# Kernel optimization log

Measured on AMD Instinct MI355X. Metric: run time of the kernel, lower is better.

## Reference

```python
import jax, jax.numpy as jnp
import numpy as np

B, S, H, N_HEAD = 2, 2048, 1024, 16
NEG = float(-(2 ** 32) + 1)  # -4294967295.0, the module's padding value
EPS = 1e-08


def setup_inputs() -> dict:
    key = jax.random.key(0)
    ks = jax.random.split(key, 11)
    sc = 0.02
    return {
        "queries": jax.random.normal(ks[0], (B, S, H), dtype=jnp.float32),
        "keys": jax.random.normal(ks[1], (B, S, H), dtype=jnp.float32),
        "values": jax.random.normal(ks[2], (B, S, H), dtype=jnp.float32),
        "Wq": jax.random.normal(ks[3], (H, H), dtype=jnp.float32) * sc,
        "bq": jax.random.normal(ks[4], (H,), dtype=jnp.float32) * sc,
        "Wk": jax.random.normal(ks[5], (H, H), dtype=jnp.float32) * sc,
        "bk": jax.random.normal(ks[6], (H,), dtype=jnp.float32) * sc,
        "Wv": jax.random.normal(ks[7], (H, H), dtype=jnp.float32) * sc,
        "bv": jax.random.normal(ks[8], (H,), dtype=jnp.float32) * sc,
        "Wo": jax.random.normal(ks[9], (H, H), dtype=jnp.float32) * sc,
        "bo": jax.random.normal(ks[10], (H,), dtype=jnp.float32) * sc,
    }


def reference(queries, keys, values, Wq, bq, Wk, bk, Wv, bv, Wo, bo):
    n = N_HEAD
    Bb, Sq, Hh = queries.shape
    Sk = keys.shape[1]
    d = Hh // n

    # Linear + ReLU projections
    Q = jax.nn.relu(queries @ Wq + bq)  # [B,Sq,H]
    K = jax.nn.relu(keys @ Wk + bk)     # [B,Sk,H]
    V = jax.nn.relu(values @ Wv + bv)   # [B,Sk,H]

    # chunk(dim=2) + cat(dim=0) == head-major split: [n,B,S,d]
    Q_ = Q.reshape(Bb, Sq, n, d).transpose(2, 0, 1, 3)
    K_ = K.reshape(Bb, Sk, n, d).transpose(2, 0, 1, 3)
    V_ = V.reshape(Bb, Sk, n, d).transpose(2, 0, 1, 3)

    # key padding mask from full (pre-chunk) K: [B,Sk]
    key_masks = jnp.sign(jnp.abs(jnp.sum(K, axis=-1)))

    # scores: [n,B,Sq,Sk], scaled by sqrt(per-head dim)
    scores = jnp.einsum("hbqd,hbkd->hbqk", Q_, K_) / (d ** 0.5)

    # multiplicative padding-mask selection -> equivalent where()
    scores = jnp.where(key_masks[None, :, None, :] == 0.0, NEG, scores)

    # causal tril mask (masked=True)
    tril = jnp.tril(jnp.ones((Sq, Sk), dtype=scores.dtype))
    scores = jnp.where(tril[None, None] == 0.0, NEG, scores)

    attn = jax.nn.softmax(scores, axis=-1)
    out = jnp.einsum("hbqk,hbkd->hbqd", attn, V_)  # [n,B,Sq,d]

    # cat chunks back along feature dim: [B,Sq,H]
    out = out.transpose(1, 2, 0, 3).reshape(Bb, Sq, Hh)

    out = jax.nn.relu(out @ Wo + bo)
    # sublayer connection (dropout treated as identity for determinism)
    out = queries + out

    # layer norm with torch-style unbiased std, gamma=1, beta=0
    mean = out.mean(axis=-1, keepdims=True)
    std = jnp.std(out, axis=-1, ddof=1, keepdims=True)
    return (out - mean) / (std + EPS)
```

## Files before the change

kernel.cpp:

```cpp
#include <hip/hip_runtime.h>
#include <math.h>

typedef __bf16 bf16;
typedef __attribute__((ext_vector_type(8))) __bf16 bf16x8;
typedef __attribute__((ext_vector_type(4))) __bf16 bf16x4;
typedef __attribute__((ext_vector_type(4))) float f32x4;

typedef __attribute__((address_space(1))) unsigned int glb_u32;
typedef __attribute__((address_space(3))) unsigned int lds_u32;

#define NEGV (-4294967295.0f)
#define SCL2 0.18033688011112042f

__device__ __forceinline__ void async_cp16(const void* g, void* l) {
  __builtin_amdgcn_global_load_lds((glb_u32*)g, (lds_u32*)l, 16, 0, 0);
}

template <int CTRL>
__device__ __forceinline__ float dppf(float x) {
  return __builtin_bit_cast(float,
      __builtin_amdgcn_mov_dpp(__builtin_bit_cast(int, x), CTRL, 0xF, 0xF, true));
}
__device__ __forceinline__ float dpp_max16(float x) {
  x = fmaxf(x, dppf<0xB1>(x));
  x = fmaxf(x, dppf<0x4E>(x));
  x = fmaxf(x, dppf<0x141>(x));
  x = fmaxf(x, dppf<0x140>(x));
  return x;
}

__global__ __launch_bounds__(256) void cvt3_kernel(
    const float* __restrict__ q, const float* __restrict__ k,
    const float* __restrict__ v, short* xq, short* xk, short* xv) {
  const int bid = blockIdx.x;
  const int which = bid >> 12;
  const int i = (bid & 4095) * 256 + threadIdx.x;
  const float* src = which == 0 ? q : (which == 1 ? k : v);
  short* dst = which == 0 ? xq : (which == 1 ? xk : xv);
  float4 vv = ((const float4*)src)[i];
  bf16x4 o;
  o[0] = (bf16)vv.x; o[1] = (bf16)vv.y; o[2] = (bf16)vv.z; o[3] = (bf16)vv.w;
  ((bf16x4*)dst)[i] = o;
}

__global__ __launch_bounds__(256) void wt_kernel(
    const float* __restrict__ W0, const float* __restrict__ W1,
    const float* __restrict__ W2, const float* __restrict__ W3,
    short* T0, short* T1, short* T2, short* T3) {
  __shared__ float tile[64][65];
  const float* W = blockIdx.z == 0 ? W0 : (blockIdx.z == 1 ? W1 : (blockIdx.z == 2 ? W2 : W3));
  bf16* T = (bf16*)(blockIdx.z == 0 ? T0 : (blockIdx.z == 1 ? T1 : (blockIdx.z == 2 ? T2 : T3)));
  const int k0 = blockIdx.y * 64, n0 = blockIdx.x * 64;
  const int tid = threadIdx.x;
  const int c = tid & 63, rr = tid >> 6;
#pragma unroll
  for (int i = 0; i < 16; i++) {
    int r = i * 4 + rr;
    tile[r][c] = W[(size_t)(k0 + r) * 1024 + n0 + c];
  }
  __syncthreads();
#pragma unroll
  for (int i = 0; i < 16; i++) {
    int r = i * 4 + rr;
    T[(size_t)(n0 + r) * 1024 + k0 + c] = (bf16)tile[c][r];
  }
}

__global__ __launch_bounds__(256) void qkv_gemm(
    const short* Xq_, const short* Xk_, const short* Xv_,
    const short* Wtq_, const short* Wtk_, const short* Wtv_,
    const float* __restrict__ bq_, const float* __restrict__ bk_, const float* __restrict__ bv_,
    short* Qo_, short* Ko_, short* Vto_) {
  __shared__ bf16 Alds[128][32];
  __shared__ bf16 Blds[128][32];
  const int f = blockIdx.x;
  const int xcd = f & 7, s = f >> 3;
  const int g = xcd + 8 * (s >> 3);
  const int which = g >> 5;
  const int m0 = (g & 31) * 128;
  const int n0 = (s & 7) * 128;
  const bf16* X  = (const bf16*)(which == 0 ? Xq_  : (which == 1 ? Xk_  : Xv_));
  const bf16* Wt = (const bf16*)(which == 0 ? Wtq_ : (which == 1 ? Wtk_ : Wtv_));
  const float* bias = which == 0 ? bq_ : (which == 1 ? bk_ : bv_);
  const int tid = threadIdx.x, wid = tid >> 6, lane = tid & 63;
  const int wr = wid >> 1, wc = wid & 1;
  const int l15 = lane & 15, lg = lane >> 4;
  const f32x4 vzero = {0.f, 0.f, 0.f, 0.f};
  f32x4 acc[4][4];
#pragma unroll
  for (int m = 0; m < 4; m++)
#pragma unroll
    for (int n = 0; n < 4; n++) acc[m][n] = vzero;

  const int sr = wid * 32 + (lane >> 2);
  const int scb = (lane & 3) * 16;

  for (int kt = 0; kt < 32; ++kt) {
    const char* ga = (const char*)(X + (size_t)(m0 + sr) * 1024 + kt * 32) + scb;
    async_cp16(ga, &Alds[wid * 32][0]);
    async_cp16(ga + 16 * 2048, &Alds[wid * 32 + 16][0]);
    const char* gb = (const char*)(Wt + (size_t)(n0 + sr) * 1024 + kt * 32) + scb;
    async_cp16(gb, &Blds[wid * 32][0]);
    async_cp16(gb + 16 * 2048, &Blds[wid * 32 + 16][0]);
    __syncthreads();
    bf16x8 a[4], bb[4];
#pragma unroll
    for (int m = 0; m < 4; m++) a[m] = *(const bf16x8*)&Alds[wr * 64 + m * 16 + l15][lg * 8];
#pragma unroll
    for (int n = 0; n < 4; n++) bb[n] = *(const bf16x8*)&Blds[wc * 64 + n * 16 + l15][lg * 8];
#pragma unroll
    for (int m = 0; m < 4; m++)
#pragma unroll
      for (int n = 0; n < 4; n++)
        acc[m][n] = __builtin_amdgcn_mfma_f32_16x16x32_bf16(a[m], bb[n], acc[m][n], 0, 0, 0);
    __syncthreads();
  }

  if (which != 2) {
    bf16* Y = (bf16*)(which == 0 ? Qo_ : Ko_);
    const float osc = (which == 0) ? SCL2 : 1.0f;
#pragma unroll
    for (int n = 0; n < 4; n++) {
      const int col = n0 + wc * 64 + n * 16 + l15;
      const float bv = bias[col];
#pragma unroll
      for (int m = 0; m < 4; m++) {
        const int row0 = m0 + wr * 64 + m * 16 + lg * 4;
#pragma unroll
        for (int r = 0; r < 4; r++) {
          float v = acc[m][n][r] + bv;
          v = v > 0.f ? v : 0.f;
          Y[(size_t)(row0 + r) * 1024 + col] = (bf16)(v * osc);
        }
      }
    }
  } else {
    bf16* Vt = (bf16*)Vto_;
#pragma unroll
    for (int n = 0; n < 4; n++) {
      const int col = n0 + wc * 64 + n * 16 + l15;
      const float bv = bias[col];
#pragma unroll
      for (int m = 0; m < 4; m++) {
        const int row0 = m0 + wr * 64 + m * 16 + lg * 4;
        const int bb2 = row0 >> 11;
        const int s2 = row0 & 2047;
        bf16x4 pk;
#pragma unroll
        for (int r = 0; r < 4; r++) {
          float v = acc[m][n][r] + bv;
          v = v > 0.f ? v : 0.f;
          pk[r] = (bf16)v;
        }
        *(bf16x4*)(Vt + ((size_t)bb2 * 1024 + col) * 2048 + s2) = pk;
      }
    }
  }
}

__global__ __launch_bounds__(256) void out_gemm(
    const short* A_, const short* Wt_, const float* __restrict__ bias,
    float* __restrict__ Y) {
  __shared__ bf16 Alds[128][32];
  __shared__ bf16 Blds[128][32];
  const bf16* X = (const bf16*)A_;
  const bf16* Wt = (const bf16*)Wt_;
  const int f = blockIdx.x;
  const int xcd = f & 7, s = f >> 3;
  const int g = xcd + 8 * (s >> 3);
  const int m0 = g * 128;
  const int n0 = (s & 7) * 128;
  const int tid = threadIdx.x, wid = tid >> 6, lane = tid & 63;
  const int wr = wid >> 1, wc = wid & 1;
  const int l15 = lane & 15, lg = lane >> 4;
  const f32x4 vzero = {0.f, 0.f, 0.f, 0.f};
  f32x4 acc[4][4];
#pragma unroll
  for (int m = 0; m < 4; m++)
#pragma unroll
    for (int n = 0; n < 4; n++) acc[m][n] = vzero;

  const int sr = wid * 32 + (lane >> 2);
  const int scb = (lane & 3) * 16;

  for (int kt = 0; kt < 32; ++kt) {
    const char* ga = (const char*)(X + (size_t)(m0 + sr) * 1024 + kt * 32) + scb;
    async_cp16(ga, &Alds[wid * 32][0]);
    async_cp16(ga + 16 * 2048, &Alds[wid * 32 + 16][0]);
    const char* gb = (const char*)(Wt + (size_t)(n0 + sr) * 1024 + kt * 32) + scb;
    async_cp16(gb, &Blds[wid * 32][0]);
    async_cp16(gb + 16 * 2048, &Blds[wid * 32 + 16][0]);
    __syncthreads();
    bf16x8 a[4], bb[4];
#pragma unroll
    for (int m = 0; m < 4; m++) a[m] = *(const bf16x8*)&Alds[wr * 64 + m * 16 + l15][lg * 8];
#pragma unroll
    for (int n = 0; n < 4; n++) bb[n] = *(const bf16x8*)&Blds[wc * 64 + n * 16 + l15][lg * 8];
#pragma unroll
    for (int m = 0; m < 4; m++)
#pragma unroll
      for (int n = 0; n < 4; n++)
        acc[m][n] = __builtin_amdgcn_mfma_f32_16x16x32_bf16(a[m], bb[n], acc[m][n], 0, 0, 0);
    __syncthreads();
  }
#pragma unroll
  for (int n = 0; n < 4; n++) {
    const int col = n0 + wc * 64 + n * 16 + l15;
    const float bv = bias[col];
#pragma unroll
    for (int m = 0; m < 4; m++) {
      const int row0 = m0 + wr * 64 + m * 16 + lg * 4;
#pragma unroll
      for (int r = 0; r < 4; r++) {
        float v = acc[m][n][r] + bv;
        Y[(size_t)(row0 + r) * 1024 + col] = v > 0.f ? v : 0.f;
      }
    }
  }
}

__global__ __launch_bounds__(256) void key_mask_kernel(const short* Kb_,
                                                       unsigned* __restrict__ kbits) {
  __shared__ unsigned bits[4];
  const bf16* Kb = (const bf16*)Kb_;
  const int wid = threadIdx.x >> 6, lane = threadIdx.x & 63;
  const int row0 = blockIdx.x * 32 + wid * 8;
  unsigned mybits = 0;
#pragma unroll
  for (int i = 0; i < 8; i++) {
    const bf16x8* p = (const bf16x8*)(Kb + (size_t)(row0 + i) * 1024);
    bf16x8 v0 = p[lane];
    bf16x8 v1 = p[64 + lane];
    float s = 0.f;
#pragma unroll
    for (int jj = 0; jj < 8; jj++) s += (float)v0[jj] + (float)v1[jj];
    for (int m = 32; m; m >>= 1) s += __shfl_xor(s, m);
    if (s != 0.f) mybits |= 1u << (wid * 8 + i);
  }
  if (lane == 0) bits[wid] = mybits;
  __syncthreads();
  if (threadIdx.x == 0) kbits[blockIdx.x] = bits[0] | bits[1] | bits[2] | bits[3];
}

__device__ __forceinline__ bf16x8 lds_read_swz(const bf16* base, int row, int cbyte) {
  return *(const bf16x8*)((const char*)base + row * 128 + (cbyte ^ ((row & 7) << 4)));
}

__global__ __launch_bounds__(128) void attn_kernel(
    const short* Q_, const short* K_, const short* Vt_,
    const unsigned* __restrict__ kbits, short* O_) {
  __shared__ bf16 Klds[2][64][64];
  __shared__ bf16 Vlds[2][64][64];
  __shared__ bf16 Plds[2][16][64];
  const bf16* Q = (const bf16*)Q_;
  const bf16* K = (const bf16*)K_;
  const bf16* Vt = (const bf16*)Vt_;
  bf16* O = (bf16*)O_;

  const int f = blockIdx.x;
  const int xcd = f & 7, idx = f >> 3;
  const int qtb = idx & 31;
  const int hb = xcd + 8 * (idx >> 5);
  const int h = hb & 15, b = hb >> 4;

  const int tid = threadIdx.x, wid = tid >> 6, lane = tid & 63;
  const int l15 = lane & 15, lg = lane >> 4;
  const f32x4 vzero = {0.f, 0.f, 0.f, 0.f};
  bf16* const pbase = &Plds[wid][0][0];

  const int srow = lane >> 3;
  const int cb = (lane & 7) * 16;
  const int cbs = cb ^ ((srow & 7) << 4);

  bf16x8 vones;
#pragma unroll
  for (int i = 0; i < 8; i++) vones[i] = (bf16)1.0f;

  for (int seg = 0; seg < 2; ++seg) {
    const int qt = (seg == 0) ? qtb : 63 - qtb;
    const int q0 = qt * 32;
    const int nkt = (32 * qt + 95) >> 6;

    const int qrow = q0 + wid * 16 + l15;
    const bf16* qp = Q + ((size_t)b * 2048 + qrow) * 1024 + h * 64;
    const bf16x8 qf0 = *(const bf16x8*)(qp + lg * 8);
    const bf16x8 qf1 = *(const bf16x8*)(qp + 32 + lg * 8);

    float Mrow[4];
    f32x4 oacc[4], oaccL;
#pragma unroll
    for (int r = 0; r < 4; r++) Mrow[r] = -INFINITY;
#pragma unroll
    for (int n = 0; n < 4; n++) oacc[n] = vzero;
    oaccL = vzero;
    float Mmin = -INFINITY;

    const char* kn = (const char*)(K + ((size_t)b * 2048 + wid * 32 + srow) * 1024 + h * 64) + cbs;
    const char* vn = (const char*)(Vt + ((size_t)b * 1024 + h * 64 + wid * 32 + srow) * 2048) + cbs;

    auto STAGE = [&](int buf) {
#pragma unroll
      for (int c = 0; c < 4; c++) {
        async_cp16(kn + c * 16384, &Klds[buf][wid * 32 + c * 8][0]);
        async_cp16(vn + c * 32768, &Vlds[buf][wid * 32 + c * 8][0]);
      }
      kn += 131072;
      vn += 128;
    };

    STAGE(0);
    __syncthreads();
    int cur = 0;
    for (int kt = 0; kt < nkt; ++kt) {
      if (kt + 1 < nkt) STAGE(cur ^ 1);

      f32x4 sacc[4];
#pragma unroll
      for (int n = 0; n < 4; n++) sacc[n] = vzero;
      {
        bf16x8 kf[4];
#pragma unroll
        for (int n = 0; n < 4; n++)
          kf[n] = lds_read_swz(&Klds[cur][0][0], n * 16 + l15, lg * 16);
        __builtin_amdgcn_s_setprio(1);
#pragma unroll
        for (int n = 0; n < 4; n++)
          sacc[n] = __builtin_amdgcn_mfma_f32_16x16x32_bf16(qf0, kf[n], sacc[n], 0, 0, 0);
        __builtin_amdgcn_s_setprio(0);
#pragma unroll
        for (int n = 0; n < 4; n++)
          kf[n] = lds_read_swz(&Klds[cur][0][0], n * 16 + l15, 64 + lg * 16);
        __builtin_amdgcn_s_setprio(1);
#pragma unroll
        for (int n = 0; n < 4; n++)
          sacc[n] = __builtin_amdgcn_mfma_f32_16x16x32_bf16(qf1, kf[n], sacc[n], 0, 0, 0);
        __builtin_amdgcn_s_setprio(0);
      }

      const unsigned w0 = kbits[b * 64 + kt * 2];
      const unsigned w1 = kbits[b * 64 + kt * 2 + 1];
      const bool last = (kt == nkt - 1);
      if (last || ((w0 & w1) != 0xFFFFFFFFu)) {
        const int qrow0 = q0 + wid * 16 + lg * 4;
#pragma unroll
        for (int n = 0; n < 4; n++) {
          const unsigned wsel = (n < 2) ? w0 : w1;
          const bool on = (wsel >> ((n & 1) * 16 + l15)) & 1;
          const int kcol = kt * 64 + n * 16 + l15;
#pragma unroll
          for (int r = 0; r < 4; r++) {
            float sc = sacc[n][r];
            if (!on) sc = NEGV;
            if (last && kcol > qrow0 + r) sc = NEGV;
            sacc[n][r] = sc;
          }
        }
      }

      {
        float lm = sacc[0][0];
#pragma unroll
        for (int n = 0; n < 4; n++)
#pragma unroll
          for (int r = 0; r < 4; r++) lm = fmaxf(lm, sacc[n][r]);
        const float gmax = dpp_max16(lm);
        if (!__all(gmax <= Mmin + 8.f)) {
#pragma unroll
          for (int r = 0; r < 4; r++) {
            float tm = fmaxf(fmaxf(sacc[0][r], sacc[1][r]), fmaxf(sacc[2][r], sacc[3][r]));
            tm = dpp_max16(tm);
            const float Mn = fmaxf(Mrow[r], tm);
            const float sc = exp2f(Mrow[r] - Mn);
            Mrow[r] = Mn;
#pragma unroll
            for (int n = 0; n < 4; n++) oacc[n][r] *= sc;
            oaccL[r] *= sc;
          }
          Mmin = fminf(fminf(Mrow[0], Mrow[1]), fminf(Mrow[2], Mrow[3]));
        }
      }

#pragma unroll
      for (int n = 0; n < 4; n++)
#pragma unroll
        for (int r = 0; r < 4; r++) {
          const float p = exp2f(sacc[n][r] - Mrow[r]);
          const int prow = lg * 4 + r;
          *(bf16*)((char*)pbase + prow * 128 +
                   (((n * 16 + l15) * 2) ^ ((prow & 7) << 4))) = (bf16)p;
        }

#pragma unroll
      for (int ks = 0; ks < 2; ks++) {
        bf16x8 vf[4];
#pragma unroll
        for (int nd = 0; nd < 4; nd++)
          vf[nd] = lds_read_swz(&Vlds[cur][0][0], nd * 16 + l15, ks * 64 + lg * 16);
        const bf16x8 pf = lds_read_swz(pbase, l15, ks * 64 + lg * 16);
        __builtin_amdgcn_s_setprio(1);
#pragma unroll
        for (int nd = 0; nd < 4; nd++)
          oacc[nd] = __builtin_amdgcn_mfma_f32_16x16x32_bf16(pf, vf[nd], oacc[nd], 0, 0, 0);
        oaccL = __builtin_amdgcn_mfma_f32_16x16x32_bf16(pf, vones, oaccL, 0, 0, 0);
        __builtin_amdgcn_s_setprio(0);
      }

      __syncthreads();
      cur ^= 1;
    }

    float inv[4];
#pragma unroll
    for (int r = 0; r < 4; r++) inv[r] = 1.0f / oaccL[r];
#pragma unroll
    for (int nd = 0; nd < 4; nd++) {
      const int col = h * 64 + nd * 16 + l15;
#pragma unroll
      for (int r = 0; r < 4; r++) {
        const float v = oacc[nd][r] * inv[r];
        O[((size_t)b * 2048 + q0 + wid * 16 + lg * 4 + r) * 1024 + col] = (bf16)v;
      }
    }
  }
}

__global__ __launch_bounds__(256) void ln_kernel(const float* __restrict__ qin,
                                                 const float* __restrict__ proj,
                                                 float* __restrict__ out) {
  __shared__ float sbuf[4];
  const int row = blockIdx.x, tid = threadIdx.x;
  const size_t base = (size_t)row * 1024 + tid * 4;
  const float4 a = *(const float4*)(qin + base);
  const float4 p = *(const float4*)(proj + base);
  const float x0 = a.x + p.x, x1 = a.y + p.y, x2 = a.z + p.z, x3 = a.w + p.w;
  float s = x0 + x1 + x2 + x3;
  for (int m = 32; m; m >>= 1) s += __shfl_xor(s, m);
  if ((tid & 63) == 0) sbuf[tid >> 6] = s;
  __syncthreads();
  s = sbuf[0] + sbuf[1] + sbuf[2] + sbuf[3];
  const float mean = s * (1.f / 1024.f);
  const float d0 = x0 - mean, d1 = x1 - mean, d2 = x2 - mean, d3 = x3 - mean;
  float ss = d0 * d0 + d1 * d1 + d2 * d2 + d3 * d3;
  __syncthreads();
  for (int m = 32; m; m >>= 1) ss += __shfl_xor(ss, m);
  if ((tid & 63) == 0) sbuf[tid >> 6] = ss;
  __syncthreads();
  ss = sbuf[0] + sbuf[1] + sbuf[2] + sbuf[3];
  const float inv = 1.f / (sqrtf(ss * (1.f / 1023.f)) + 1e-8f);
  float4 o;
  o.x = d0 * inv; o.y = d1 * inv; o.z = d2 * inv; o.w = d3 * inv;
  *(float4*)(out + base) = o;
}

extern "C" void kernel_launch(void* const* d_in, const int* in_sizes, int n_in,
                              void* d_out, int out_size, void* d_ws, size_t ws_size,
                              hipStream_t stream) {
  (void)in_sizes; (void)n_in; (void)out_size; (void)ws_size;
  const float* queries = (const float*)d_in[0];
  const float* keys    = (const float*)d_in[1];
  const float* values  = (const float*)d_in[2];
  const float* Wq = (const float*)d_in[3];  const float* bq = (const float*)d_in[4];
  const float* Wk = (const float*)d_in[5];  const float* bk = (const float*)d_in[6];
  const float* Wv = (const float*)d_in[7];  const float* bv = (const float*)d_in[8];
  const float* Wo = (const float*)d_in[9];  const float* bo = (const float*)d_in[10];
  float* out = (float*)d_out;

  char* w = (char*)d_ws;
  const size_t SZ_X = (size_t)4096 * 1024 * 2;
  const size_t SZ_W = (size_t)1024 * 1024 * 2;
  short* Xq  = (short*)w; w += SZ_X;
  short* Xk  = (short*)w; w += SZ_X;
  short* Xv  = (short*)w; w += SZ_X;
  short* Wtq = (short*)w; w += SZ_W;
  short* Wtk = (short*)w; w += SZ_W;
  short* Wtv = (short*)w; w += SZ_W;
  short* Wto = (short*)w; w += SZ_W;
  short* Qb  = (short*)w; w += SZ_X;
  short* Kb  = (short*)w; w += SZ_X;
  short* Vtb = (short*)w; w += SZ_X;
  short* Ab  = (short*)w; w += SZ_X;
  unsigned* kbits = (unsigned*)w; w += 4096;
  float* proj = (float*)w; w += (size_t)4096 * 1024 * 4;

  cvt3_kernel<<<12288, 256, 0, stream>>>(queries, keys, values, Xq, Xk, Xv);
  wt_kernel<<<dim3(16, 16, 4), 256, 0, stream>>>(Wq, Wk, Wv, Wo, Wtq, Wtk, Wtv, Wto);
  qkv_gemm<<<768, 256, 0, stream>>>(Xq, Xk, Xv, Wtq, Wtk, Wtv,
                                    bq, bk, bv, Qb, Kb, Vtb);
  key_mask_kernel<<<128, 256, 0, stream>>>(Kb, kbits);
  attn_kernel<<<1024, 128, 0, stream>>>(Qb, Kb, Vtb, kbits, Ab);
  out_gemm<<<256, 256, 0, stream>>>(Ab, Wto, bo, proj);
  ln_kernel<<<4096, 256, 0, stream>>>(queries, proj, out);
}
```

Measured before the change: 160.5 us.

## Fuse fp32-to-bf16 input conversion into QKV GEMM and store projection as bf16

```diff
diff --git a/kernel.cpp b/kernel.cpp
--- a/kernel.cpp
+++ b/kernel.cpp
@@ -27,20 +27,6 @@
   x = fmaxf(x, dppf<0x141>(x));
   x = fmaxf(x, dppf<0x140>(x));
   return x;
-}
-
-__global__ __launch_bounds__(256) void cvt3_kernel(
-    const float* __restrict__ q, const float* __restrict__ k,
-    const float* __restrict__ v, short* xq, short* xk, short* xv) {
-  const int bid = blockIdx.x;
-  const int which = bid >> 12;
-  const int i = (bid & 4095) * 256 + threadIdx.x;
-  const float* src = which == 0 ? q : (which == 1 ? k : v);
-  short* dst = which == 0 ? xq : (which == 1 ? xk : xv);
-  float4 vv = ((const float4*)src)[i];
-  bf16x4 o;
-  o[0] = (bf16)vv.x; o[1] = (bf16)vv.y; o[2] = (bf16)vv.z; o[3] = (bf16)vv.w;
-  ((bf16x4*)dst)[i] = o;
 }
 
 __global__ __launch_bounds__(256) void wt_kernel(
@@ -67,21 +53,115 @@
 }
 
 __global__ __launch_bounds__(256) void qkv_gemm(
-    const short* Xq_, const short* Xk_, const short* Xv_,
+    const float* __restrict__ Xq, const float* __restrict__ Xk,
+    const float* __restrict__ Xv,
     const short* Wtq_, const short* Wtk_, const short* Wtv_,
     const float* __restrict__ bq_, const float* __restrict__ bk_, const float* __restrict__ bv_,
     short* Qo_, short* Ko_, short* Vto_) {
+  __shared__ float Af[128][32];
+  __shared__ bf16 Blds[128][32];
+  const int which = blockIdx.z;
+  const float* X = which == 0 ? Xq : (which == 1 ? Xk : Xv);
+  const bf16* Wt = (const bf16*)(which == 0 ? Wtq_ : (which == 1 ? Wtk_ : Wtv_));
+  const float* bias = which == 0 ? bq_ : (which == 1 ? bk_ : bv_);
+  const int m0 = blockIdx.y * 128, n0 = blockIdx.x * 128;
+  const int tid = threadIdx.x, wid = tid >> 6, lane = tid & 63;
+  const int wr = wid >> 1, wc = wid & 1;
+  const int l15 = lane & 15, lg = lane >> 4;
+  const f32x4 vzero = {0.f, 0.f, 0.f, 0.f};
+  f32x4 acc[4][4];
+#pragma unroll
+  for (int m = 0; m < 4; m++)
+#pragma unroll
+    for (int n = 0; n < 4; n++) acc[m][n] = vzero;
+
+  const int asrow = lane >> 3;
+  const int acbs = ((lane & 7) * 16) ^ ((asrow & 7) << 4);
+  const int bsr = wid * 32 + (lane >> 2);
+  const int bscb = (lane & 3) * 16;
+
+  for (int kt = 0; kt < 32; ++kt) {
+#pragma unroll
+    for (int c = 0; c < 4; c++) {
+      const char* ga = (const char*)(X + (size_t)(m0 + wid * 32 + c * 8 + asrow) * 1024 + kt * 32) + acbs;
+      async_cp16(ga, &Af[wid * 32 + c * 8][0]);
+    }
+    const char* gb = (const char*)(Wt + (size_t)(n0 + bsr) * 1024 + kt * 32) + bscb;
+    async_cp16(gb, &Blds[wid * 32][0]);
+    async_cp16(gb + 16 * 2048, &Blds[wid * 32 + 16][0]);
+    __syncthreads();
+    bf16x8 a[4], bb[4];
+#pragma unroll
+    for (int m = 0; m < 4; m++) {
+      const int row = wr * 64 + m * 16 + l15;
+      const int swz = (row & 7) << 4;
+      const char* ar = (const char*)&Af[0][0] + row * 128;
+      const float4 f0 = *(const float4*)(ar + ((lg * 32) ^ swz));
+      const float4 f1 = *(const float4*)(ar + ((lg * 32 + 16) ^ swz));
+      a[m][0] = (bf16)f0.x; a[m][1] = (bf16)f0.y; a[m][2] = (bf16)f0.z; a[m][3] = (bf16)f0.w;
+      a[m][4] = (bf16)f1.x; a[m][5] = (bf16)f1.y; a[m][6] = (bf16)f1.z; a[m][7] = (bf16)f1.w;
+    }
+#pragma unroll
+    for (int n = 0; n < 4; n++) bb[n] = *(const bf16x8*)&Blds[wc * 64 + n * 16 + l15][lg * 8];
+#pragma unroll
+    for (int m = 0; m < 4; m++)
+#pragma unroll
+      for (int n = 0; n < 4; n++)
+        acc[m][n] = __builtin_amdgcn_mfma_f32_16x16x32_bf16(a[m], bb[n], acc[m][n], 0, 0, 0);
+    __syncthreads();
+  }
+
+  if (which != 2) {
+    bf16* Y = (bf16*)(which == 0 ? Qo_ : Ko_);
+    const float osc = (which == 0) ? SCL2 : 1.0f;
+#pragma unroll
+    for (int n = 0; n < 4; n++) {
+      const int col = n0 + wc * 64 + n * 16 + l15;
+      const float bv = bias[col];
+#pragma unroll
+      for (int m = 0; m < 4; m++) {
+        const int row0 = m0 + wr * 64 + m * 16 + lg * 4;
+#pragma unroll
+        for (int r = 0; r < 4; r++) {
+          float v = acc[m][n][r] + bv;
+          v = v > 0.f ? v : 0.f;
+          Y[(size_t)(row0 + r) * 1024 + col] = (bf16)(v * osc);
+        }
+      }
+    }
+  } else {
+    bf16* Vt = (bf16*)Vto_;
+#pragma unroll
+    for (int n = 0; n < 4; n++) {
+      const int col = n0 + wc * 64 + n * 16 + l15;
+      const float bv = bias[col];
+#pragma unroll
+      for (int m = 0; m < 4; m++) {
+        const int row0 = m0 + wr * 64 + m * 16 + lg * 4;
+        const int bb2 = row0 >> 11;
+        const int s2 = row0 & 2047;
+        bf16x4 pk;
+#pragma unroll
+        for (int r = 0; r < 4; r++) {
+          float v = acc[m][n][r] + bv;
+          v = v > 0.f ? v : 0.f;
+          pk[r] = (bf16)v;
+        }
+        *(bf16x4*)(Vt + ((size_t)bb2 * 1024 + col) * 2048 + s2) = pk;
+      }
+    }
+  }
+}
+
+__global__ __launch_bounds__(256) void out_gemm(
+    const short* A_, const short* Wt_, const float* __restrict__ bias,
+    short* __restrict__ Y_) {
   __shared__ bf16 Alds[128][32];
   __shared__ bf16 Blds[128][32];
-  const int f = blockIdx.x;
-  const int xcd = f & 7, s = f >> 3;
-  const int g = xcd + 8 * (s >> 3);
-  const int which = g >> 5;
-  const int m0 = (g & 31) * 128;
-  const int n0 = (s & 7) * 128;
-  const bf16* X  = (const bf16*)(which == 0 ? Xq_  : (which == 1 ? Xk_  : Xv_));
-  const bf16* Wt = (const bf16*)(which == 0 ? Wtq_ : (which == 1 ? Wtk_ : Wtv_));
-  const float* bias = which == 0 ? bq_ : (which == 1 ? bk_ : bv_);
+  const bf16* X = (const bf16*)A_;
+  const bf16* Wt = (const bf16*)Wt_;
+  bf16* Y = (bf16*)Y_;
+  const int m0 = blockIdx.y * 128, n0 = blockIdx.x * 128;
   const int tid = threadIdx.x, wid = tid >> 6, lane = tid & 63;
   const int wr = wid >> 1, wc = wid & 1;
   const int l15 = lane & 15, lg = lane >> 4;
@@ -115,94 +195,6 @@
         acc[m][n] = __builtin_amdgcn_mfma_f32_16x16x32_bf16(a[m], bb[n], acc[m][n], 0, 0, 0);
     __syncthreads();
   }
-
-  if (which != 2) {
-    bf16* Y = (bf16*)(which == 0 ? Qo_ : Ko_);
-    const float osc = (which == 0) ? SCL2 : 1.0f;
-#pragma unroll
-    for (int n = 0; n < 4; n++) {
-      const int col = n0 + wc * 64 + n * 16 + l15;
-      const float bv = bias[col];
-#pragma unroll
-      for (int m = 0; m < 4; m++) {
-        const int row0 = m0 + wr * 64 + m * 16 + lg * 4;
-#pragma unroll
-        for (int r = 0; r < 4; r++) {
-          float v = acc[m][n][r] + bv;
-          v = v > 0.f ? v : 0.f;
-          Y[(size_t)(row0 + r) * 1024 + col] = (bf16)(v * osc);
-        }
-      }
-    }
-  } else {
-    bf16* Vt = (bf16*)Vto_;
-#pragma unroll
-    for (int n = 0; n < 4; n++) {
-      const int col = n0 + wc * 64 + n * 16 + l15;
-      const float bv = bias[col];
-#pragma unroll
-      for (int m = 0; m < 4; m++) {
-        const int row0 = m0 + wr * 64 + m * 16 + lg * 4;
-        const int bb2 = row0 >> 11;
-        const int s2 = row0 & 2047;
-        bf16x4 pk;
-#pragma unroll
-        for (int r = 0; r < 4; r++) {
-          float v = acc[m][n][r] + bv;
-          v = v > 0.f ? v : 0.f;
-          pk[r] = (bf16)v;
-        }
-        *(bf16x4*)(Vt + ((size_t)bb2 * 1024 + col) * 2048 + s2) = pk;
-      }
-    }
-  }
-}
-
-__global__ __launch_bounds__(256) void out_gemm(
-    const short* A_, const short* Wt_, const float* __restrict__ bias,
-    float* __restrict__ Y) {
-  __shared__ bf16 Alds[128][32];
-  __shared__ bf16 Blds[128][32];
-  const bf16* X = (const bf16*)A_;
-  const bf16* Wt = (const bf16*)Wt_;
-  const int f = blockIdx.x;
-  const int xcd = f & 7, s = f >> 3;
-  const int g = xcd + 8 * (s >> 3);
-  const int m0 = g * 128;
-  const int n0 = (s & 7) * 128;
-  const int tid = threadIdx.x, wid = tid >> 6, lane = tid & 63;
-  const int wr = wid >> 1, wc = wid & 1;
-  const int l15 = lane & 15, lg = lane >> 4;
-  const f32x4 vzero = {0.f, 0.f, 0.f, 0.f};
-  f32x4 acc[4][4];
-#pragma unroll
-  for (int m = 0; m < 4; m++)
-#pragma unroll
-    for (int n = 0; n < 4; n++) acc[m][n] = vzero;
-
-  const int sr = wid * 32 + (lane >> 2);
-  const int scb = (lane & 3) * 16;
-
-  for (int kt = 0; kt < 32; ++kt) {
-    const char* ga = (const char*)(X + (size_t)(m0 + sr) * 1024 + kt * 32) + scb;
-    async_cp16(ga, &Alds[wid * 32][0]);
-    async_cp16(ga + 16 * 2048, &Alds[wid * 32 + 16][0]);
-    const char* gb = (const char*)(Wt + (size_t)(n0 + sr) * 1024 + kt * 32) + scb;
-    async_cp16(gb, &Blds[wid * 32][0]);
-    async_cp16(gb + 16 * 2048, &Blds[wid * 32 + 16][0]);
-    __syncthreads();
-    bf16x8 a[4], bb[4];
-#pragma unroll
-    for (int m = 0; m < 4; m++) a[m] = *(const bf16x8*)&Alds[wr * 64 + m * 16 + l15][lg * 8];
-#pragma unroll
-    for (int n = 0; n < 4; n++) bb[n] = *(const bf16x8*)&Blds[wc * 64 + n * 16 + l15][lg * 8];
-#pragma unroll
-    for (int m = 0; m < 4; m++)
-#pragma unroll
-      for (int n = 0; n < 4; n++)
-        acc[m][n] = __builtin_amdgcn_mfma_f32_16x16x32_bf16(a[m], bb[n], acc[m][n], 0, 0, 0);
-    __syncthreads();
-  }
 #pragma unroll
   for (int n = 0; n < 4; n++) {
     const int col = n0 + wc * 64 + n * 16 + l15;
@@ -213,7 +205,7 @@
 #pragma unroll
       for (int r = 0; r < 4; r++) {
         float v = acc[m][n][r] + bv;
-        Y[(size_t)(row0 + r) * 1024 + col] = v > 0.f ? v : 0.f;
+        Y[(size_t)(row0 + r) * 1024 + col] = (bf16)(v > 0.f ? v : 0.f);
       }
     }
   }
@@ -425,14 +417,16 @@
 }
 
 __global__ __launch_bounds__(256) void ln_kernel(const float* __restrict__ qin,
-                                                 const float* __restrict__ proj,
+                                                 const short* __restrict__ proj_,
                                                  float* __restrict__ out) {
   __shared__ float sbuf[4];
+  const bf16* proj = (const bf16*)proj_;
   const int row = blockIdx.x, tid = threadIdx.x;
   const size_t base = (size_t)row * 1024 + tid * 4;
   const float4 a = *(const float4*)(qin + base);
-  const float4 p = *(const float4*)(proj + base);
-  const float x0 = a.x + p.x, x1 = a.y + p.y, x2 = a.z + p.z, x3 = a.w + p.w;
+  const bf16x4 pb = *(const bf16x4*)(proj + base);
+  const float x0 = a.x + (float)pb[0], x1 = a.y + (float)pb[1];
+  const float x2 = a.z + (float)pb[2], x3 = a.w + (float)pb[3];
   float s = x0 + x1 + x2 + x3;
   for (int m = 32; m; m >>= 1) s += __shfl_xor(s, m);
   if ((tid & 63) == 0) sbuf[tid >> 6] = s;
@@ -468,9 +462,6 @@
   char* w = (char*)d_ws;
   const size_t SZ_X = (size_t)4096 * 1024 * 2;
   const size_t SZ_W = (size_t)1024 * 1024 * 2;
-  short* Xq  = (short*)w; w += SZ_X;
-  short* Xk  = (short*)w; w += SZ_X;
-  short* Xv  = (short*)w; w += SZ_X;
   short* Wtq = (short*)w; w += SZ_W;
   short* Wtk = (short*)w; w += SZ_W;
   short* Wtv = (short*)w; w += SZ_W;
@@ -479,15 +470,15 @@
   short* Kb  = (short*)w; w += SZ_X;
   short* Vtb = (short*)w; w += SZ_X;
   short* Ab  = (short*)w; w += SZ_X;
+  short* proj = (short*)w; w += SZ_X;
   unsigned* kbits = (unsigned*)w; w += 4096;
-  float* proj = (float*)w; w += (size_t)4096 * 1024 * 4;
-
-  cvt3_kernel<<<12288, 256, 0, stream>>>(queries, keys, values, Xq, Xk, Xv);
+
   wt_kernel<<<dim3(16, 16, 4), 256, 0, stream>>>(Wq, Wk, Wv, Wo, Wtq, Wtk, Wtv, Wto);
-  qkv_gemm<<<768, 256, 0, stream>>>(Xq, Xk, Xv, Wtq, Wtk, Wtv,
-                                    bq, bk, bv, Qb, Kb, Vtb);
+  qkv_gemm<<<dim3(8, 32, 3), 256, 0, stream>>>(queries, keys, values,
+                                               Wtq, Wtk, Wtv,
+                                               bq, bk, bv, Qb, Kb, Vtb);
   key_mask_kernel<<<128, 256, 0, stream>>>(Kb, kbits);
   attn_kernel<<<1024, 128, 0, stream>>>(Qb, Kb, Vtb, kbits, Ab);
-  out_gemm<<<256, 256, 0, stream>>>(Ab, Wto, bo, proj);
+  out_gemm<<<dim3(8, 32), 256, 0, stream>>>(Ab, Wto, bo, proj);
   ln_kernel<<<4096, 256, 0, stream>>>(queries, proj, out);
 }
```

After: 166.0 us. 1.03x slower.
